# Performance work log

Hardware: AMD Instinct MI355X
Metric: run time of the kernel (lower is better)

## Reference

```python
import jax, jax.numpy as jnp
import numpy as np

N = 8192   # number of points (p) == number of reference points (r); must match for final bmm
D = 1024   # feature width of the Linear projections


def setup_inputs() -> dict:
    key = jax.random.key(0)
    ks = jax.random.split(key, 8)
    s = 1.0 / np.sqrt(D)
    return {
        "p": jax.random.normal(ks[0], (N, D), dtype=jnp.float32),
        "r": jax.random.normal(ks[1], (N, D), dtype=jnp.float32),
        "Wh": jax.random.uniform(ks[2], (D, D), jnp.float32, -s, s),
        "bh": jax.random.uniform(ks[3], (D,), jnp.float32, -s, s),
        "Wl": jax.random.uniform(ks[4], (D, D), jnp.float32, -s, s),
        "bl": jax.random.uniform(ks[5], (D,), jnp.float32, -s, s),
        "Wg": jax.random.uniform(ks[6], (D, D), jnp.float32, -s, s),
        "bg": jax.random.uniform(ks[7], (D,), jnp.float32, -s, s),
    }


def reference(p, r, Wh, bh, Wl, bl, Wg, bg):
    # Linear projections (torch Linear: x @ W.T + b)
    q = p @ Wh.T + bh          # [N, D]  M_h(p)
    k = r @ Wl.T + bl          # [N, D]  M_l(r)
    v = p @ Wg.T + bg          # [N, D]  M_g(p)
    scores = q @ k.T           # [N, N]  == bmm(q[None], k[None].transpose(1,2))[0]
    # torch softmax dim=1 on [1, N, N] normalizes over the QUERY axis -> axis=0 here
    attn = jax.nn.softmax(scores, axis=0)
    return p + attn @ v        # residual add
```

## Files before the change

### kernel.cpp

```cpp
#include <hip/hip_runtime.h>
#include <hip/hip_fp16.h>

typedef _Float16 f16;
typedef __attribute__((ext_vector_type(8))) _Float16 f16x8;
typedef __attribute__((ext_vector_type(4))) float f32x4;

#define NPTS 8192
#define DIM  1024
#define HL2E 0.721347520444482f
#define S2SHIFT 50.0f
#define TBUF (128 * 32)

__device__ __forceinline__ void glds16(const void* g, void* l) {
  __builtin_amdgcn_global_load_lds(
      (const __attribute__((address_space(1))) void*)g,
      (__attribute__((address_space(3))) void*)l, 16, 0, 0);
}


__global__ void cvt_f32_f16(const float* __restrict__ src, f16* __restrict__ dst, int n) {
  int i = (blockIdx.x * 256 + threadIdx.x) * 8;
  if (i >= n) return;
  const float4* s = (const float4*)(src + i);
  float4 a = s[0], b = s[1];
  f16x8 o;
  o[0] = (f16)a.x; o[1] = (f16)a.y; o[2] = (f16)a.z; o[3] = (f16)a.w;
  o[4] = (f16)b.x; o[5] = (f16)b.y; o[6] = (f16)b.z; o[7] = (f16)b.w;
  *(f16x8*)(dst + i) = o;
}

__global__ void zero_f32(float* __restrict__ p, int n) {
  int i = blockIdx.x * 256 + threadIdx.x;
  if (i < n) p[i] = 0.f;
}

__global__ void mk_scales(const float* __restrict__ colsum,
                          f16* __restrict__ ics2, f16* __restrict__ ics4) {
  int j = blockIdx.x * 256 + threadIdx.x;
  float r2 = rsqrtf(colsum[j]);
  ics2[j] = (f16)r2;
  ics4[j] = (f16)sqrtf(r2);
}

__global__ void vscale(f16* __restrict__ vt, const f16* __restrict__ ics2) {
  long i = ((long)blockIdx.x * 256 + threadIdx.x) * 8;
  f16x8 v = *(f16x8*)(vt + i);
  f16x8 s = *(const f16x8*)(ics2 + (i & (NPTS - 1)));
  *(f16x8*)(vt + i) = v * s;
}

__global__ __launch_bounds__(256, 2)
void proj_fused(const f16* __restrict__ p_h, const f16* __restrict__ r_h,
                const f16* __restrict__ Wh, const f16* __restrict__ Wl,
                const f16* __restrict__ Wg,
                const float* __restrict__ bh, const float* __restrict__ bl,
                const float* __restrict__ bg,
                f16* __restrict__ q_h, f16* __restrict__ k_h,
                f16* __restrict__ vt_h) {
  __shared__ f16 sA[2 * TBUF];
  __shared__ f16 sB[2 * TBUF];
  const int sub = blockIdx.x >> 9;
  const int bl_ = blockIdx.x & 511;
  const long bi = (long)(bl_ & 63) * 128;
  const long bj = (long)(bl_ >> 6) * 128;
  const f16* A = (sub == 1) ? r_h : p_h;
  const f16* B = (sub == 0) ? Wh : (sub == 1) ? Wl : Wg;
  const float* bias = (sub == 0) ? bh : (sub == 1) ? bl : bg;

  const int t = threadIdx.x;
  const int w = t >> 6, l = t & 63;
  const int wm = (w >> 1) * 64, wn = (w & 1) * 64;
  const int lr = l & 15;
  const int fbase = lr * 32 + (((l >> 4) ^ ((lr >> 1) & 3)) * 8);
  const int grow = w * 16 + (l >> 2);
  const int gcol = ((l & 3) ^ ((l >> 3) & 3)) * 8;
  const f16* gA = A + (bi + grow) * (long)DIM + gcol;
  const f16* gB = B + (bj + grow) * (long)DIM + gcol;
  const int lw0 = (w * 16) * 32, lw1 = (64 + w * 16) * 32;

  glds16(gA, sA + lw0);
  glds16(gA + 64l * DIM, sA + lw1);
  glds16(gB, sB + lw0);
  glds16(gB + 64l * DIM, sB + lw1);
  gA += 32; gB += 32;

  f32x4 acc[4][4] = {};
  const int nk = DIM / 32;
  for (int k = 0; k < nk; k++) {
    const int cur = (k & 1) * TBUF, nxt = TBUF - cur;
    __syncthreads();
    if (k + 1 < nk) {
      glds16(gA, sA + nxt + lw0);
      glds16(gA + 64l * DIM, sA + nxt + lw1);
      glds16(gB, sB + nxt + lw0);
      glds16(gB + 64l * DIM, sB + nxt + lw1);
      gA += 32; gB += 32;
    }
    f16x8 af[4], bf[4];
#pragma unroll
    for (int mt = 0; mt < 4; mt++)
      af[mt] = *(const f16x8*)(sA + cur + (wm + mt * 16) * 32 + fbase);
#pragma unroll
    for (int nt = 0; nt < 4; nt++)
      bf[nt] = *(const f16x8*)(sB + cur + (wn + nt * 16) * 32 + fbase);
#pragma unroll
    for (int mt = 0; mt < 4; mt++)
#pragma unroll
      for (int nt = 0; nt < 4; nt++)
        acc[mt][nt] = __builtin_amdgcn_mfma_f32_16x16x32_f16(af[mt], bf[nt], acc[mt][nt], 0, 0, 0);
  }

  const int rbase = (l >> 4) * 4;
  f16* C = (sub == 0) ? q_h : (sub == 1) ? k_h : vt_h;
#pragma unroll
  for (int nt = 0; nt < 4; nt++) {
    const long col = bj + wn + nt * 16 + lr;
    const float bb = bias[col];
#pragma unroll
    for (int mt = 0; mt < 4; mt++) {
      const long row0 = bi + wm + mt * 16 + rbase;
      if (sub < 2) {
#pragma unroll
        for (int g = 0; g < 4; g++)
          C[(row0 + g) * DIM + col] = (f16)(acc[mt][nt][g] + bb);
      } else {
        union { unsigned long long u; f16 h[4]; } pk;
#pragma unroll
        for (int g = 0; g < 4; g++) pk.h[g] = (f16)(acc[mt][nt][g] + bb);
        *(unsigned long long*)(C + col * (long)NPTS + row0) = pk.u;
      }
    }
  }
}

__global__ __launch_bounds__(256, 2)
void gemm_qk(const f16* __restrict__ A, const f16* __restrict__ B,
             f16* __restrict__ S, float* __restrict__ colsum) {
  __shared__ f16 sA[2 * TBUF];
  __shared__ f16 sB[2 * TBUF];
  const long bi = (long)blockIdx.y * 128;
  const long bj = (long)blockIdx.x * 128;
  const int t = threadIdx.x;
  const int w = t >> 6, l = t & 63;
  const int wm = (w >> 1) * 64, wn = (w & 1) * 64;
  const int lr = l & 15;
  const int fbase = lr * 32 + (((l >> 4) ^ ((lr >> 1) & 3)) * 8);
  const int grow = w * 16 + (l >> 2);
  const int gcol = ((l & 3) ^ ((l >> 3) & 3)) * 8;
  const f16* gA = A + (bi + grow) * (long)DIM + gcol;
  const f16* gB = B + (bj + grow) * (long)DIM + gcol;
  const int lw0 = (w * 16) * 32, lw1 = (64 + w * 16) * 32;

  glds16(gA, sA + lw0);
  glds16(gA + 64l * DIM, sA + lw1);
  glds16(gB, sB + lw0);
  glds16(gB + 64l * DIM, sB + lw1);
  gA += 32; gB += 32;

  f32x4 acc[4][4] = {};
  const int nk = DIM / 32;
  for (int k = 0; k < nk; k++) {
    const int cur = (k & 1) * TBUF, nxt = TBUF - cur;
    __syncthreads();
    if (k + 1 < nk) {
      glds16(gA, sA + nxt + lw0);
      glds16(gA + 64l * DIM, sA + nxt + lw1);
      glds16(gB, sB + nxt + lw0);
      glds16(gB + 64l * DIM, sB + nxt + lw1);
      gA += 32; gB += 32;
    }
    f16x8 af[4], bf[4];
#pragma unroll
    for (int mt = 0; mt < 4; mt++)
      af[mt] = *(const f16x8*)(sA + cur + (wm + mt * 16) * 32 + fbase);
#pragma unroll
    for (int nt = 0; nt < 4; nt++)
      bf[nt] = *(const f16x8*)(sB + cur + (wn + nt * 16) * 32 + fbase);
#pragma unroll
    for (int mt = 0; mt < 4; mt++)
#pragma unroll
      for (int nt = 0; nt < 4; nt++)
        acc[mt][nt] = __builtin_amdgcn_mfma_f32_16x16x32_f16(af[mt], bf[nt], acc[mt][nt], 0, 0, 0);
  }

  const int rbase = (l >> 4) * 4;
#pragma unroll
  for (int nt = 0; nt < 4; nt++) {
    const long col = bj + wn + nt * 16 + lr;
    float csum = 0.f;
#pragma unroll
    for (int mt = 0; mt < 4; mt++) {
      const long row0 = bi + wm + mt * 16 + rbase;
#pragma unroll
      for (int g = 0; g < 4; g++) {
        float e = exp2f((acc[mt][nt][g] - S2SHIFT) * HL2E);
        e = fminf(e, 240.f);
        f16 eh = (f16)e;
        S[(row0 + g) * NPTS + col] = eh;
        float ef = (float)eh;
        csum += ef * ef;
      }
    }
    csum += __shfl_xor(csum, 16);
    csum += __shfl_xor(csum, 32);
    if (l < 16) atomicAdd(colsum + col, csum);
  }
}

__global__ __launch_bounds__(256, 2)
void gemm_pv(const f16* __restrict__ Sm, const f16* __restrict__ vt,
             const f16* __restrict__ ics4, const float* __restrict__ Res,
             float* __restrict__ out) {
  __shared__ f16 sA[2 * TBUF];
  __shared__ f16 sB[2 * TBUF];
  const long bi = (long)(blockIdx.x & 63) * 128;
  const long bj = (long)(blockIdx.x >> 6) * 128;

  const int t = threadIdx.x;
  const int w = t >> 6, l = t & 63;
  const int wm = (w >> 1) * 64, wn = (w & 1) * 64;
  const int lr = l & 15;
  const int fbase = lr * 32 + (((l >> 4) ^ ((lr >> 1) & 3)) * 8);
  const int grow = w * 16 + (l >> 2);
  const int gcol = ((l & 3) ^ ((l >> 3) & 3)) * 8;
  const f16* gB = vt + (bj + grow) * (long)NPTS + gcol;
  const int lw0 = (w * 16) * 32, lw1 = (64 + w * 16) * 32;

  const int sr = t >> 2, sc = (t & 3) * 8;
  const int ssw = ((t & 3) ^ ((t >> 3) & 3)) * 8;
  const f16* gAs = Sm + (bi + sr) * (long)NPTS + sc;
  const f16* gIc = ics4 + sc;
  f16x8 ra0, ra1, icv;

  const int nk = NPTS / 32;

  ra0 = *(const f16x8*)gAs;
  ra1 = *(const f16x8*)(gAs + 64l * NPTS);
  icv = *(const f16x8*)gIc;
  {
    f16x8 t0 = ra0 * icv; t0 = t0 * t0;
    f16x8 t1 = ra1 * icv; t1 = t1 * t1;
    *(f16x8*)(sA + sr * 32 + ssw) = t0;
    *(f16x8*)(sA + (sr + 64) * 32 + ssw) = t1;
  }
  gAs += 32; gIc += 32;
  ra0 = *(const f16x8*)gAs;
  ra1 = *(const f16x8*)(gAs + 64l * NPTS);
  icv = *(const f16x8*)gIc;
  glds16(gB, sB + lw0);
  glds16(gB + 64l * NPTS, sB + lw1);
  gB += 32;

  f32x4 acc[4][4] = {};
  for (int k = 0; k < nk; k++) {
    const int cur = (k & 1) * TBUF, nxt = TBUF - cur;
    __syncthreads();
    if (k + 1 < nk) {
      f16x8 t0 = ra0 * icv; t0 = t0 * t0;
      f16x8 t1 = ra1 * icv; t1 = t1 * t1;
      *(f16x8*)(sA + nxt + sr * 32 + ssw) = t0;
      *(f16x8*)(sA + nxt + (sr + 64) * 32 + ssw) = t1;
      if (k + 2 < nk) {
        gAs += 32; gIc += 32;
        ra0 = *(const f16x8*)gAs;
        ra1 = *(const f16x8*)(gAs + 64l * NPTS);
        icv = *(const f16x8*)gIc;
      }
      glds16(gB, sB + nxt + lw0);
      glds16(gB + 64l * NPTS, sB + nxt + lw1);
      gB += 32;
    }
    f16x8 af[4], bf[4];
#pragma unroll
    for (int mt = 0; mt < 4; mt++)
      af[mt] = *(const f16x8*)(sA + cur + (wm + mt * 16) * 32 + fbase);
#pragma unroll
    for (int nt = 0; nt < 4; nt++)
      bf[nt] = *(const f16x8*)(sB + cur + (wn + nt * 16) * 32 + fbase);
#pragma unroll
    for (int mt = 0; mt < 4; mt++)
#pragma unroll
      for (int nt = 0; nt < 4; nt++)
        acc[mt][nt] = __builtin_amdgcn_mfma_f32_16x16x32_f16(af[mt], bf[nt], acc[mt][nt], 0, 0, 0);
  }

  const int rbase = (l >> 4) * 4;
#pragma unroll
  for (int nt = 0; nt < 4; nt++) {
    const long col = bj + wn + nt * 16 + lr;
#pragma unroll
    for (int mt = 0; mt < 4; mt++) {
      const long row0 = bi + wm + mt * 16 + rbase;
#pragma unroll
      for (int g = 0; g < 4; g++)
        out[(row0 + g) * DIM + col] = acc[mt][nt][g] + Res[(row0 + g) * (long)DIM + col];
    }
  }
}

extern "C" void kernel_launch(void* const* d_in, const int* in_sizes, int n_in,
                              void* d_out, int out_size, void* d_ws, size_t ws_size,
                              hipStream_t stream) {
  const float* p  = (const float*)d_in[0];
  const float* r  = (const float*)d_in[1];
  const float* Wh = (const float*)d_in[2];
  const float* bh = (const float*)d_in[3];
  const float* Wl = (const float*)d_in[4];
  const float* bl = (const float*)d_in[5];
  const float* Wg = (const float*)d_in[6];
  const float* bg = (const float*)d_in[7];
  float* out = (float*)d_out;

  char* ws = (char*)d_ws;
  f16* q_h  = (f16*)(ws + (0ull  << 20));
  f16* k_h  = (f16*)(ws + (16ull << 20));
  f16* vt_h = (f16*)(ws + (32ull << 20));
  f16* p_h  = (f16*)(ws + (48ull << 20));
  f16* r_h  = (f16*)(ws + (64ull << 20));
  f16* wh_h = (f16*)(ws + (80ull << 20));
  f16* wl_h = (f16*)(ws + (82ull << 20));
  f16* wg_h = (f16*)(ws + (84ull << 20));
  f16* S    = (f16*)(ws + (96ull << 20));
  float* colsum = (float*)(ws + (224ull << 20));
  f16* ics2 = (f16*)(ws + (225ull << 20));
  f16* ics4 = (f16*)(ws + (226ull << 20));

  const int nP = NPTS * DIM, nW = DIM * DIM;
  cvt_f32_f16<<<nP / 2048, 256, 0, stream>>>(p,  p_h,  nP);
  cvt_f32_f16<<<nP / 2048, 256, 0, stream>>>(r,  r_h,  nP);
  cvt_f32_f16<<<nW / 2048, 256, 0, stream>>>(Wh, wh_h, nW);
  cvt_f32_f16<<<nW / 2048, 256, 0, stream>>>(Wl, wl_h, nW);
  cvt_f32_f16<<<nW / 2048, 256, 0, stream>>>(Wg, wg_h, nW);
  zero_f32<<<NPTS / 256, 256, 0, stream>>>(colsum, NPTS);

  dim3 blk(256);
  proj_fused<<<1536, blk, 0, stream>>>(p_h, r_h, wh_h, wl_h, wg_h,
                                       bh, bl, bg, q_h, k_h, vt_h);
  gemm_qk<<<dim3(64, 64), blk, 0, stream>>>(q_h, k_h, S, colsum);
  mk_scales<<<NPTS / 256, 256, 0, stream>>>(colsum, ics2, ics4);
  vscale<<<(NPTS / 8) * (DIM / 256), 256, 0, stream>>>(vt_h, ics2);
  gemm_pv<<<512, blk, 0, stream>>>(S, vt_h, ics4, p, out);
}
```

Before: 583.5 us.

## Split-K the PV GEMM into two halves and swizzle QK block order

The PV GEMM now splits its 8192-long reduction into two halves, launching 1024 blocks instead of 512 so more of the GPU's compute units are busy. Each half writes fp32 partial sums to scratch, and a new reduce kernel adds both partials to the residual. Separately, the QK GEMM grid is flattened and remapped into 8x8 block groups to improve L2 reuse of the q/k tiles. The trade-off is an extra 2x32MB of fp32 partial writes and reads plus one more launch. The partial buffers reuse the q/k/p_h workspace regions, which are dead by this point.

```diff
diff --git a/kernel.cpp b/kernel.cpp
--- a/kernel.cpp
+++ b/kernel.cpp
@@ -47,6 +47,18 @@
   f16x8 v = *(f16x8*)(vt + i);
   f16x8 s = *(const f16x8*)(ics2 + (i & (NPTS - 1)));
   *(f16x8*)(vt + i) = v * s;
+}
+
+__global__ void reduce_out(const float* __restrict__ p,
+                           const float* __restrict__ pa,
+                           const float* __restrict__ pb,
+                           float* __restrict__ out) {
+  long i = ((long)blockIdx.x * 256 + threadIdx.x) * 4;
+  float4 a = *(const float4*)(p + i);
+  float4 b = *(const float4*)(pa + i);
+  float4 c = *(const float4*)(pb + i);
+  a.x += b.x + c.x; a.y += b.y + c.y; a.z += b.z + c.z; a.w += b.w + c.w;
+  *(float4*)(out + i) = a;
 }
 
 __global__ __launch_bounds__(256, 2)
@@ -138,8 +150,13 @@
              f16* __restrict__ S, float* __restrict__ colsum) {
   __shared__ f16 sA[2 * TBUF];
   __shared__ f16 sB[2 * TBUF];
-  const long bi = (long)blockIdx.y * 128;
-  const long bj = (long)blockIdx.x * 128;
+  const int b = blockIdx.x;
+  const int sx = b & 7;
+  const int j = b >> 3;
+  const int st = j >> 6;
+  const int wi = j & 63;
+  const long bi = (long)(st * 8 + (wi >> 3)) * 128;
+  const long bj = (long)(sx * 8 + (wi & 7)) * 128;
   const int t = threadIdx.x;
   const int w = t >> 6, l = t & 63;
   const int wm = (w >> 1) * 64, wn = (w & 1) * 64;
@@ -209,12 +226,15 @@
 
 __global__ __launch_bounds__(256, 2)
 void gemm_pv(const f16* __restrict__ Sm, const f16* __restrict__ vt,
-             const f16* __restrict__ ics4, const float* __restrict__ Res,
-             float* __restrict__ out) {
+             const f16* __restrict__ ics4,
+             float* __restrict__ part0, float* __restrict__ part1) {
   __shared__ f16 sA[2 * TBUF];
   __shared__ f16 sB[2 * TBUF];
-  const long bi = (long)(blockIdx.x & 63) * 128;
-  const long bj = (long)(blockIdx.x >> 6) * 128;
+  const int split = blockIdx.x >> 9;
+  const int bl_ = blockIdx.x & 511;
+  const long bi = (long)(bl_ & 63) * 128;
+  const long bj = (long)(bl_ >> 6) * 128;
+  const long koff = (long)split * (NPTS / 2);
 
   const int t = threadIdx.x;
   const int w = t >> 6, l = t & 63;
@@ -223,16 +243,16 @@
   const int fbase = lr * 32 + (((l >> 4) ^ ((lr >> 1) & 3)) * 8);
   const int grow = w * 16 + (l >> 2);
   const int gcol = ((l & 3) ^ ((l >> 3) & 3)) * 8;
-  const f16* gB = vt + (bj + grow) * (long)NPTS + gcol;
+  const f16* gB = vt + (bj + grow) * (long)NPTS + koff + gcol;
   const int lw0 = (w * 16) * 32, lw1 = (64 + w * 16) * 32;
 
   const int sr = t >> 2, sc = (t & 3) * 8;
   const int ssw = ((t & 3) ^ ((t >> 3) & 3)) * 8;
-  const f16* gAs = Sm + (bi + sr) * (long)NPTS + sc;
-  const f16* gIc = ics4 + sc;
+  const f16* gAs = Sm + (bi + sr) * (long)NPTS + koff + sc;
+  const f16* gIc = ics4 + koff + sc;
   f16x8 ra0, ra1, icv;
 
-  const int nk = NPTS / 32;
+  const int nk = (NPTS / 2) / 32;
 
   ra0 = *(const f16x8*)gAs;
   ra1 = *(const f16x8*)(gAs + 64l * NPTS);
@@ -284,6 +304,7 @@
         acc[mt][nt] = __builtin_amdgcn_mfma_f32_16x16x32_f16(af[mt], bf[nt], acc[mt][nt], 0, 0, 0);
   }
 
+  float* part = split ? part1 : part0;
   const int rbase = (l >> 4) * 4;
 #pragma unroll
   for (int nt = 0; nt < 4; nt++) {
@@ -293,7 +314,7 @@
       const long row0 = bi + wm + mt * 16 + rbase;
 #pragma unroll
       for (int g = 0; g < 4; g++)
-        out[(row0 + g) * DIM + col] = acc[mt][nt][g] + Res[(row0 + g) * (long)DIM + col];
+        part[(row0 + g) * DIM + col] = acc[mt][nt][g];
     }
   }
 }
@@ -324,6 +345,8 @@
   float* colsum = (float*)(ws + (224ull << 20));
   f16* ics2 = (f16*)(ws + (225ull << 20));
   f16* ics4 = (f16*)(ws + (226ull << 20));
+  float* part0 = (float*)(ws + (0ull  << 20));
+  float* part1 = (float*)(ws + (48ull << 20));
 
   const int nP = NPTS * DIM, nW = DIM * DIM;
   cvt_f32_f16<<<nP / 2048, 256, 0, stream>>>(p,  p_h,  nP);
@@ -336,8 +359,9 @@
   dim3 blk(256);
   proj_fused<<<1536, blk, 0, stream>>>(p_h, r_h, wh_h, wl_h, wg_h,
                                        bh, bl, bg, q_h, k_h, vt_h);
-  gemm_qk<<<dim3(64, 64), blk, 0, stream>>>(q_h, k_h, S, colsum);
+  gemm_qk<<<4096, blk, 0, stream>>>(q_h, k_h, S, colsum);
   mk_scales<<<NPTS / 256, 256, 0, stream>>>(colsum, ics2, ics4);
   vscale<<<(NPTS / 8) * (DIM / 256), 256, 0, stream>>>(vt_h, ics2);
-  gemm_pv<<<512, blk, 0, stream>>>(S, vt_h, ics4, p, out);
-}
+  gemm_pv<<<1024, blk, 0, stream>>>(S, vt_h, ics4, part0, part1);
+  reduce_out<<<nP / 1024, 256, 0, stream>>>(p, part0, part1, out);
+}
```

Measured after the change: 540.7 us. 7.3% less time.
